# Optimization experiments

Measured on AMD Instinct MI355X. Metric: run time of the kernel, lower is better.

## Reference

```python
import jax, jax.numpy as jnp
import numpy as np
import math

NC = 80
STRIDES = [8.0, 16.0, 32.0]
BALANCE = [4.0, 1.0, 0.4]
BOX_W, OBJ_W, CLS_W = 7.5, 1.0, 0.5
B = 32
NT = 400


def build_targets(shapes, targets):
    """NumPy port of YOLOv11Loss.build_targets (na=1). Pure index/label
    construction -> depends only on shapes + ground-truth, no grads."""
    nt = targets.shape[0]
    ai = np.zeros((1, nt, 1), dtype=np.float32)  # na=1 anchor ids
    t_all = np.concatenate([targets[None].astype(np.float32), ai], axis=2)  # [1,nt,7]
    g = 0.5
    off = np.array([[0, 0], [1, 0], [0, 1], [-1, 0], [0, -1]], dtype=np.float32) * g
    out = []
    for i, shape in enumerate(shapes):
        anchor = float(STRIDES[i])
        H, W = shape[2], shape[3]
        gain = np.array([1, 1, W, H, W, H, 1], dtype=np.float32)
        t = t_all * gain  # [1,nt,7] in grid units
        r = t[..., 4:6] / anchor
        keep = np.maximum(r, 1.0 / r).max(axis=2) < 4.0  # [1,nt]
        t = t[keep]  # [n,7]
        gxy = t[:, 2:4]
        gxi = np.array([W, H], dtype=np.float32) - gxy
        jj, kk = ((gxy % 1 < g) & (gxy > 1)).T
        ll, mm = ((gxi % 1 < g) & (gxi > 1)).T
        J = np.stack([np.ones_like(jj), jj, kk, ll, mm])  # [5,n]
        t = np.tile(t[None], (5, 1, 1))[J]  # [m,7]
        offsets = (np.zeros_like(gxy)[None] + off[:, None])[J]  # [m,2]
        b = t[:, 0].astype(np.int64)
        c = t[:, 1].astype(np.int64)
        gxy = t[:, 2:4]
        gwh = t[:, 4:6]
        a = t[:, 6].astype(np.int64)
        gij = (gxy - offsets).astype(np.int64)  # trunc toward 0, matches .long()
        gi = np.clip(gij[:, 0], 0, W - 1)
        gj = np.clip(gij[:, 1], 0, H - 1)
        gij_c = np.stack([gi, gj], axis=1)  # torch clamps in-place before tbox
        tbox = np.concatenate([gxy - gij_c, gwh], axis=1).astype(np.float32)
        out.append((b, a, gj, gi, tbox, c))
    return out


def ciou(pbox, tbox, eps=1e-7):
    """Elementwise CIoU on [n,4] xywh boxes (matches bbox_iou(..., CIoU=True))."""
    px, py, pw, ph = pbox[:, 0], pbox[:, 1], pbox[:, 2], pbox[:, 3]
    tx, ty, tw, th = tbox[:, 0], tbox[:, 1], tbox[:, 2], tbox[:, 3]
    b1x1, b1x2 = px - pw / 2, px + pw / 2
    b1y1, b1y2 = py - ph / 2, py + ph / 2
    b2x1, b2x2 = tx - tw / 2, tx + tw / 2
    b2y1, b2y2 = ty - th / 2, ty + th / 2
    inter = jnp.clip(jnp.minimum(b1x2, b2x2) - jnp.maximum(b1x1, b2x1), 0) * \
            jnp.clip(jnp.minimum(b1y2, b2y2) - jnp.maximum(b1y1, b2y1), 0)
    union = pw * ph + tw * th - inter + eps
    iou = inter / union
    cw = jnp.maximum(b1x2, b2x2) - jnp.minimum(b1x1, b2x1)
    ch = jnp.maximum(b1y2, b2y2) - jnp.minimum(b1y1, b2y1)
    c2 = cw ** 2 + ch ** 2 + eps
    rho2 = ((b2x1 + b2x2 - b1x1 - b1x2) ** 2 + (b2y1 + b2y2 - b1y1 - b1y2) ** 2) / 4
    v = (4.0 / math.pi ** 2) * (jnp.arctan(tw / th) - jnp.arctan(pw / ph)) ** 2
    alpha = jax.lax.stop_gradient(v / (v - iou + (1 + eps)))
    return iou - (rho2 / c2 + v * alpha)


def bce_mean(logits, targets):
    # BCEWithLogitsLoss(pos_weight=1), mean reduction: softplus(x) - x*z
    return jnp.mean(jax.nn.softplus(logits) - logits * targets)


def setup_inputs() -> dict:
    key = jax.random.key(0)
    k0, k1, k2 = jax.random.split(key, 3)
    p0 = jax.random.normal(k0, (B, 1, 80, 80, NC + 5), dtype=jnp.float32)
    p1 = jax.random.normal(k1, (B, 1, 40, 40, NC + 5), dtype=jnp.float32)
    p2 = jax.random.normal(k2, (B, 1, 20, 20, NC + 5), dtype=jnp.float32)
    rng = np.random.default_rng(0)
    bidx = rng.integers(0, B, NT).astype(np.float32)
    cls = rng.integers(0, NC, NT).astype(np.float32)
    xy = rng.uniform(0.05, 0.95, (NT, 2)).astype(np.float32)
    wh = rng.uniform(0.05, 0.5, (NT, 2)).astype(np.float32)
    targets = jnp.asarray(np.concatenate([bidx[:, None], cls[:, None], xy, wh], axis=1))
    return {"p0": p0, "p1": p1, "p2": p2, "targets": targets}


def reference(p0, p1, p2, targets):
    preds = [p0, p1, p2]
    bt = build_targets([p.shape for p in preds], np.asarray(targets))
    lbox = jnp.zeros((), jnp.float32)
    lobj = jnp.zeros((), jnp.float32)
    lcls = jnp.zeros((), jnp.float32)
    for i, p in enumerate(preds):
        b, a, gj, gi, tb, tc = bt[i]
        tobj = jnp.zeros(p.shape[:4], p.dtype)
        n = b.shape[0]
        if n:
            pred = p[b, a, gj, gi]  # [n, nc+5] gather
            pxy = jax.nn.sigmoid(pred[:, :2]) * 2.0 - 0.5
            pwh = (jax.nn.sigmoid(pred[:, 2:4]) * 2.0) ** 2 * STRIDES[i]
            pbox = jnp.concatenate([pxy, pwh], axis=1)
            iou = ciou(pbox, jnp.asarray(tb))
            lbox = lbox + jnp.mean(1.0 - iou)
            iou_d = jax.lax.stop_gradient(jnp.clip(iou, 0.0)).astype(p.dtype)
            tobj = tobj.at[b, a, gj, gi].set(iou_d)  # scatter objectness targets
            pcls = pred[:, 5:]
            tmat = jnp.zeros((n, NC), p.dtype).at[np.arange(n), tc].set(1.0)
            lcls = lcls + bce_mean(pcls, tmat)
        lobj = lobj + bce_mean(p[..., 4], tobj) * BALANCE[i]
    lbox = lbox * BOX_W
    lobj = lobj * OBJ_W
    lcls = lcls * CLS_W
    bs = preds[0].shape[0]
    loss = (lbox + lobj + lcls) * bs
    comps = jax.lax.stop_gradient(jnp.stack([lbox, lobj, lcls]))
    return loss, comps
```

## Files before the change

### kernel.cpp

```cpp
#include <hip/hip_runtime.h>

#define NCLS 80
#define BATCH 32
#define N0 (BATCH * 80 * 80)
#define N1 (BATCH * 40 * 40)
#define N2 (BATCH * 20 * 20)
#define NCELL (N0 + N1 + N2)
#define NFLT (NCELL * (NCLS + 5))
#define NF4  (NFLT / 4)
#define L0F4 ((N0 * (NCLS + 5)) / 4)
#define L01F4 (((N0 + N1) * (NCLS + 5)) / 4)
#define TPB 256
#define WPB (TPB / 64)
#define STREAM_BLOCKS 2048
#define STRIDE4 (STREAM_BLOCKS * TPB)
#define NBMAX 2400

__device__ float g_part[NBMAX * 12];

__device__ __forceinline__ float sigmoid_f(float x) {
    return 1.0f / (1.0f + expf(-x));
}

__device__ __forceinline__ float softplus_f(float x) {
    return fmaxf(x, 0.0f) + log1pf(expf(-fabsf(x)));
}

__device__ __forceinline__ float ciou_f(float px, float py, float pw, float ph,
                                        float tx, float ty, float tw, float th) {
    const float eps = 1e-7f;
    float b1x1 = px - pw * 0.5f, b1x2 = px + pw * 0.5f;
    float b1y1 = py - ph * 0.5f, b1y2 = py + ph * 0.5f;
    float b2x1 = tx - tw * 0.5f, b2x2 = tx + tw * 0.5f;
    float b2y1 = ty - th * 0.5f, b2y2 = ty + th * 0.5f;
    float iw = fmaxf(fminf(b1x2, b2x2) - fmaxf(b1x1, b2x1), 0.0f);
    float ih = fmaxf(fminf(b1y2, b2y2) - fmaxf(b1y1, b2y1), 0.0f);
    float inter = iw * ih;
    float uni = pw * ph + tw * th - inter + eps;
    float iou = inter / uni;
    float cw = fmaxf(b1x2, b2x2) - fminf(b1x1, b2x1);
    float ch = fmaxf(b1y2, b2y2) - fminf(b1y1, b2y1);
    float c2 = cw * cw + ch * ch + eps;
    float dx = b2x1 + b2x2 - b1x1 - b1x2;
    float dy = b2y1 + b2y2 - b1y1 - b1y2;
    float rho2 = (dx * dx + dy * dy) * 0.25f;
    float dat = atanf(tw / th) - atanf(pw / ph);
    const float k = 0.40528473456935108577551785f;
    float v = k * dat * dat;
    float alpha = v / (v - iou + (1.0f + eps));
    return iou - (rho2 / c2 + v * alpha);
}

__device__ __forceinline__ void stream_body(
        const float4* __restrict__ f0, const float4* __restrict__ f1,
        const float4* __restrict__ f2, int i4, unsigned int r,
        float& acc0, float& acc1, float& acc2) {
    const float4* src;
    int off, lvl;
    if (i4 < L0F4)       { src = f0; off = i4;         lvl = 0; }
    else if (i4 < L01F4) { src = f1; off = i4 - L0F4;  lvl = 1; }
    else                 { src = f2; off = i4 - L01F4; lvl = 2; }
    float4 v = src[off];
    unsigned int j = 4u - r;
    float x = (j == 0u) ? v.x : (j == 1u) ? v.y : (j == 2u) ? v.z : v.w;
    float maskf = (r >= 1u && r <= 4u) ? 1.0f : 0.0f;
    float sp = maskf * softplus_f(x);
    acc0 += (lvl == 0) ? sp : 0.0f;
    acc1 += (lvl == 1) ? sp : 0.0f;
    acc2 += (lvl == 2) ? sp : 0.0f;
}

__global__ __launch_bounds__(TPB) void main_kernel(
        const float* __restrict__ p0,
        const float* __restrict__ p1,
        const float* __restrict__ p2,
        const float* __restrict__ tg, int nt, int tgtBlocks) {
    __shared__ float sh[12];
    int tid = threadIdx.x;
    if (tid < 12) sh[tid] = 0.0f;
    __syncthreads();

    if ((int)blockIdx.x >= tgtBlocks) {
        const float4* f0 = (const float4*)p0;
        const float4* f1 = (const float4*)p1;
        const float4* f2 = (const float4*)p2;
        int i4 = (blockIdx.x - tgtBlocks) * TPB + tid;
        unsigned int r = ((unsigned int)i4 * 4u) % 85u;
        float acc0 = 0.0f, acc1 = 0.0f, acc2 = 0.0f;
        while (i4 + 3 * STRIDE4 < NF4) {
            unsigned int r0 = r;
            unsigned int r1 = r0 + 32u; if (r1 >= 85u) r1 -= 85u;
            unsigned int r2 = r1 + 32u; if (r2 >= 85u) r2 -= 85u;
            unsigned int r3 = r2 + 32u; if (r3 >= 85u) r3 -= 85u;
            stream_body(f0, f1, f2, i4,               r0, acc0, acc1, acc2);
            stream_body(f0, f1, f2, i4 + STRIDE4,     r1, acc0, acc1, acc2);
            stream_body(f0, f1, f2, i4 + 2 * STRIDE4, r2, acc0, acc1, acc2);
            stream_body(f0, f1, f2, i4 + 3 * STRIDE4, r3, acc0, acc1, acc2);
            r = r3 + 32u; if (r >= 85u) r -= 85u;
            i4 += 4 * STRIDE4;
        }
        while (i4 < NF4) {
            stream_body(f0, f1, f2, i4, r, acc0, acc1, acc2);
            r += 32u; if (r >= 85u) r -= 85u;
            i4 += STRIDE4;
        }
        #pragma unroll
        for (int off = 32; off > 0; off >>= 1) {
            acc0 += __shfl_down(acc0, off, 64);
            acc1 += __shfl_down(acc1, off, 64);
            acc2 += __shfl_down(acc2, off, 64);
        }
        if ((tid & 63) == 0) {
            atomicAdd(&sh[9], acc0);
            atomicAdd(&sh[10], acc1);
            atomicAdd(&sh[11], acc2);
        }
    } else {
        int lane = tid & 63;
        int wtask = blockIdx.x * WPB + (tid >> 6);
        if (wtask < 3 * nt) {
            int lvl = wtask / nt;
            int t = wtask - lvl * nt;

            int W = (lvl == 0) ? 80 : ((lvl == 1) ? 40 : 20);
            float s = (lvl == 0) ? 8.0f : ((lvl == 1) ? 16.0f : 32.0f);
            const float* p = (lvl == 0) ? p0 : ((lvl == 1) ? p1 : p2);

            const float* row = tg + t * 6;
            float bf = row[0], cf = row[1];
            float x = row[2], y = row[3], w = row[4], h = row[5];

            float Wf = (float)W;
            float gw = w * Wf, gh = h * Wf;
            float rw = gw / s, rh = gh / s;
            float m = fmaxf(fmaxf(rw, 1.0f / rw), fmaxf(rh, 1.0f / rh));
            if (m < 4.0f) {
                float gx = x * Wf, gy = y * Wf;
                int b = (int)bf;
                int c = (int)cf;

                float ox[3], oy[3];
                int ne = 0;
                ox[ne] = 0.0f; oy[ne] = 0.0f; ne++;
                bool jj = (fmodf(gx, 1.0f) < 0.5f) && (gx > 1.0f);
                bool kk = (fmodf(gy, 1.0f) < 0.5f) && (gy > 1.0f);
                float gxi = Wf - gx, gyi = Wf - gy;
                bool ll = (fmodf(gxi, 1.0f) < 0.5f) && (gxi > 1.0f);
                bool mm = (fmodf(gyi, 1.0f) < 0.5f) && (gyi > 1.0f);
                if (jj) { ox[ne] = 0.5f;  oy[ne] = 0.0f;  ne++; }
                if (ll) { ox[ne] = -0.5f; oy[ne] = 0.0f;  ne++; }
                if (kk) { ox[ne] = 0.0f;  oy[ne] = 0.5f;  ne++; }
                if (mm) { ox[ne] = 0.0f;  oy[ne] = -0.5f; ne++; }

                float cls_lane = 0.0f;
                float lbox_u = 0.0f, lobj_u = 0.0f;
                int hot = 5 + c;
                for (int e = 0; e < ne; e++) {
                    int gi = (int)(gx - ox[e]);
                    int gj = (int)(gy - oy[e]);
                    gi = min(max(gi, 0), W - 1);
                    gj = min(max(gj, 0), W - 1);
                    int cell = (b * W + gj) * W + gi;
                    const float* pr = p + (size_t)cell * (NCLS + 5);

                    float v1 = pr[lane];
                    float v2 = (lane < 21) ? pr[64 + lane] : 0.0f;

                    float c0 = __shfl(v1, 0, 64);
                    float c1 = __shfl(v1, 1, 64);
                    float c2 = __shfl(v1, 2, 64);
                    float c3 = __shfl(v1, 3, 64);
                    float c4 = __shfl(v1, 4, 64);

                    float px = sigmoid_f(c0) * 2.0f - 0.5f;
                    float py = sigmoid_f(c1) * 2.0f - 0.5f;
                    float sw = sigmoid_f(c2) * 2.0f;
                    float shh = sigmoid_f(c3) * 2.0f;
                    float pw = sw * sw * s;
                    float ph = shh * shh * s;

                    float tbx = gx - (float)gi;
                    float tby = gy - (float)gj;

                    float iou = ciou_f(px, py, pw, ph, tbx, tby, gw, gh);
                    lbox_u += 1.0f - iou;
                    lobj_u += c4 * fmaxf(iou, 0.0f);

                    float s1 = (lane >= 5) ? softplus_f(v1) : 0.0f;
                    float s2 = (lane < 21) ? softplus_f(v2) : 0.0f;
                    cls_lane += s1 + s2;
                    if (hot < 64) { if (lane == hot)      cls_lane -= v1; }
                    else          { if (lane == hot - 64) cls_lane -= v2; }
                }
                #pragma unroll
                for (int off = 32; off > 0; off >>= 1)
                    cls_lane += __shfl_down(cls_lane, off, 64);
                if (lane == 0) {
                    atomicAdd(&sh[lvl], lbox_u);
                    atomicAdd(&sh[3 + lvl], cls_lane);
                    atomicAdd(&sh[6 + lvl], (float)ne);
                    atomicAdd(&sh[9 + lvl], -lobj_u);
                }
            }
        }
    }
    __syncthreads();
    if (tid < 12) g_part[blockIdx.x * 12 + tid] = sh[tid];
}

__global__ __launch_bounds__(TPB) void reduce_kernel(float* __restrict__ out,
                                                     int nblk) {
    __shared__ float red[12][TPB];
    int tid = threadIdx.x;
    float loc[12];
    #pragma unroll
    for (int c = 0; c < 12; c++) loc[c] = 0.0f;
    const float4* gp4 = (const float4*)g_part;
    for (int b = tid; b < nblk; b += TPB) {
        float4 a = gp4[b * 3];
        float4 bb = gp4[b * 3 + 1];
        float4 cc = gp4[b * 3 + 2];
        loc[0] += a.x;  loc[1] += a.y;  loc[2] += a.z;  loc[3] += a.w;
        loc[4] += bb.x; loc[5] += bb.y; loc[6] += bb.z; loc[7] += bb.w;
        loc[8] += cc.x; loc[9] += cc.y; loc[10] += cc.z; loc[11] += cc.w;
    }
    #pragma unroll
    for (int c = 0; c < 12; c++) red[c][tid] = loc[c];
    __syncthreads();
    for (int st = TPB / 2; st > 0; st >>= 1) {
        if (tid < st) {
            #pragma unroll
            for (int c = 0; c < 12; c++) red[c][tid] += red[c][tid + st];
        }
        __syncthreads();
    }
    if (tid == 0) {
        const float BAL[3] = {4.0f, 1.0f, 0.4f};
        const float NCF[3] = {(float)N0, (float)N1, (float)N2};
        float lbox = 0.0f, lcls = 0.0f, lobj = 0.0f;
        for (int l = 0; l < 3; l++) {
            float n = red[6 + l][0];
            if (n > 0.5f) {
                lbox += red[l][0] / n;
                lcls += red[3 + l][0] / (n * (float)NCLS);
            }
            lobj += red[9 + l][0] / NCF[l] * BAL[l];
        }
        lbox *= 7.5f;
        lcls *= 0.5f;
        float loss = (lbox + lobj + lcls) * (float)BATCH;
        out[0] = loss;
        out[1] = lbox;
        out[2] = lobj;
        out[3] = lcls;
    }
}

extern "C" void kernel_launch(void* const* d_in, const int* in_sizes, int n_in,
                              void* d_out, int out_size, void* d_ws, size_t ws_size,
                              hipStream_t stream) {
    const float* p0 = (const float*)d_in[0];
    const float* p1 = (const float*)d_in[1];
    const float* p2 = (const float*)d_in[2];
    const float* tg = (const float*)d_in[3];
    int nt = in_sizes[3] / 6;
    float* out = (float*)d_out;

    int nWaveTasks = 3 * nt;
    int tgtBlocks = (nWaveTasks + WPB - 1) / WPB;
    if (tgtBlocks > NBMAX - STREAM_BLOCKS) tgtBlocks = NBMAX - STREAM_BLOCKS;
    int nblk = tgtBlocks + STREAM_BLOCKS;

    main_kernel<<<nblk, TPB, 0, stream>>>(p0, p1, p2, tg, nt, tgtBlocks);
    reduce_kernel<<<1, TPB, 0, stream>>>(out, nblk);
}
```

Baseline: 128.2 us.

## Fuse final reduction into main kernel via last-block counter and deepen unroll

The separate single-block reduce kernel is removed. Each block now increments a global done counter after writing its partials, and the last block to finish performs the final 12-way reduction and resets the counter. This saves one kernel launch and its dependency gap. The streaming loop is also unrolled from 4 to 8 independent loads per iteration to keep more memory requests in flight. In exchange, every block pays for an extra atomic and fence, and the shared reduction array adds LDS use to every block, which may lower occupancy.

```diff
diff --git a/kernel.cpp b/kernel.cpp
--- a/kernel.cpp
+++ b/kernel.cpp
@@ -17,6 +17,7 @@
 #define NBMAX 2400
 
 __device__ float g_part[NBMAX * 12];
+__device__ int g_done;
 
 __device__ __forceinline__ float sigmoid_f(float x) {
     return 1.0f / (1.0f + expf(-x));
@@ -74,8 +75,10 @@
         const float* __restrict__ p0,
         const float* __restrict__ p1,
         const float* __restrict__ p2,
-        const float* __restrict__ tg, int nt, int tgtBlocks) {
+        const float* __restrict__ tg, int nt, int tgtBlocks, int nblk,
+        float* __restrict__ out) {
     __shared__ float sh[12];
+    __shared__ int lastFlag;
     int tid = threadIdx.x;
     if (tid < 12) sh[tid] = 0.0f;
     __syncthreads();
@@ -87,17 +90,20 @@
         int i4 = (blockIdx.x - tgtBlocks) * TPB + tid;
         unsigned int r = ((unsigned int)i4 * 4u) % 85u;
         float acc0 = 0.0f, acc1 = 0.0f, acc2 = 0.0f;
-        while (i4 + 3 * STRIDE4 < NF4) {
-            unsigned int r0 = r;
-            unsigned int r1 = r0 + 32u; if (r1 >= 85u) r1 -= 85u;
-            unsigned int r2 = r1 + 32u; if (r2 >= 85u) r2 -= 85u;
-            unsigned int r3 = r2 + 32u; if (r3 >= 85u) r3 -= 85u;
-            stream_body(f0, f1, f2, i4,               r0, acc0, acc1, acc2);
-            stream_body(f0, f1, f2, i4 + STRIDE4,     r1, acc0, acc1, acc2);
-            stream_body(f0, f1, f2, i4 + 2 * STRIDE4, r2, acc0, acc1, acc2);
-            stream_body(f0, f1, f2, i4 + 3 * STRIDE4, r3, acc0, acc1, acc2);
-            r = r3 + 32u; if (r >= 85u) r -= 85u;
-            i4 += 4 * STRIDE4;
+        while (i4 + 7 * STRIDE4 < NF4) {
+            unsigned int rr[8];
+            rr[0] = r;
+            #pragma unroll
+            for (int u = 1; u < 8; u++) {
+                rr[u] = rr[u - 1] + 32u;
+                if (rr[u] >= 85u) rr[u] -= 85u;
+            }
+            #pragma unroll
+            for (int u = 0; u < 8; u++)
+                stream_body(f0, f1, f2, i4 + u * STRIDE4, rr[u],
+                            acc0, acc1, acc2);
+            r = rr[7] + 32u; if (r >= 85u) r -= 85u;
+            i4 += 8 * STRIDE4;
         }
         while (i4 < NF4) {
             stream_body(f0, f1, f2, i4, r, acc0, acc1, acc2);
@@ -206,12 +212,17 @@
     }
     __syncthreads();
     if (tid < 12) g_part[blockIdx.x * 12 + tid] = sh[tid];
-}
-
-__global__ __launch_bounds__(TPB) void reduce_kernel(float* __restrict__ out,
-                                                     int nblk) {
+
+    if (tid == 0) {
+        __threadfence();
+        int old = atomicAdd(&g_done, 1);
+        lastFlag = (old == nblk - 1);
+    }
+    __syncthreads();
+    if (!lastFlag) return;
+    __threadfence();
+
     __shared__ float red[12][TPB];
-    int tid = threadIdx.x;
     float loc[12];
     #pragma unroll
     for (int c = 0; c < 12; c++) loc[c] = 0.0f;
@@ -253,6 +264,7 @@
         out[1] = lbox;
         out[2] = lobj;
         out[3] = lcls;
+        g_done = 0;
     }
 }
 
@@ -271,6 +283,6 @@
     if (tgtBlocks > NBMAX - STREAM_BLOCKS) tgtBlocks = NBMAX - STREAM_BLOCKS;
     int nblk = tgtBlocks + STREAM_BLOCKS;
 
-    main_kernel<<<nblk, TPB, 0, stream>>>(p0, p1, p2, tg, nt, tgtBlocks);
-    reduce_kernel<<<1, TPB, 0, stream>>>(out, nblk);
-}
+    main_kernel<<<nblk, TPB, 0, stream>>>(p0, p1, p2, tg, nt, tgtBlocks, nblk,
+                                          out);
+}
```

Result: slower. 205.0 us (+59.9%).

## Gather only objectness logits instead of streaming the whole prediction tensor

Applied to the files above, without the earlier changes.

Replaces the grid-stride float4 stream over every prediction value, where only channel 4 was used, with one thread per grid cell that loads just the objectness logit at stride 85. It then applies softplus, does a wave reduction and adds the result to that level's shared accumulator. This is meant to cut DRAM traffic, since only the cache lines holding objectness values are fetched. In exchange the loads are strided and uncoalesced, and the grid size is now fixed by the cell count. NBMAX is lowered to fit the new block count.

```diff
diff --git a/kernel.cpp b/kernel.cpp
--- a/kernel.cpp
+++ b/kernel.cpp
@@ -5,16 +5,12 @@
 #define N0 (BATCH * 80 * 80)
 #define N1 (BATCH * 40 * 40)
 #define N2 (BATCH * 20 * 20)
-#define NCELL (N0 + N1 + N2)
-#define NFLT (NCELL * (NCLS + 5))
-#define NF4  (NFLT / 4)
-#define L0F4 ((N0 * (NCLS + 5)) / 4)
-#define L01F4 (((N0 + N1) * (NCLS + 5)) / 4)
 #define TPB 256
 #define WPB (TPB / 64)
-#define STREAM_BLOCKS 2048
-#define STRIDE4 (STREAM_BLOCKS * TPB)
-#define NBMAX 2400
+#define OBJ_BLOCKS ((N0 + N1 + N2) / TPB)
+#define OBJ_B0 (N0 / TPB)
+#define OBJ_B01 ((N0 + N1) / TPB)
+#define NBMAX 1500
 
 __device__ float g_part[NBMAX * 12];
 
@@ -51,25 +47,6 @@
     return iou - (rho2 / c2 + v * alpha);
 }
 
-__device__ __forceinline__ void stream_body(
-        const float4* __restrict__ f0, const float4* __restrict__ f1,
-        const float4* __restrict__ f2, int i4, unsigned int r,
-        float& acc0, float& acc1, float& acc2) {
-    const float4* src;
-    int off, lvl;
-    if (i4 < L0F4)       { src = f0; off = i4;         lvl = 0; }
-    else if (i4 < L01F4) { src = f1; off = i4 - L0F4;  lvl = 1; }
-    else                 { src = f2; off = i4 - L01F4; lvl = 2; }
-    float4 v = src[off];
-    unsigned int j = 4u - r;
-    float x = (j == 0u) ? v.x : (j == 1u) ? v.y : (j == 2u) ? v.z : v.w;
-    float maskf = (r >= 1u && r <= 4u) ? 1.0f : 0.0f;
-    float sp = maskf * softplus_f(x);
-    acc0 += (lvl == 0) ? sp : 0.0f;
-    acc1 += (lvl == 1) ? sp : 0.0f;
-    acc2 += (lvl == 2) ? sp : 0.0f;
-}
-
 __global__ __launch_bounds__(TPB) void main_kernel(
         const float* __restrict__ p0,
         const float* __restrict__ p1,
@@ -81,40 +58,19 @@
     __syncthreads();
 
     if ((int)blockIdx.x >= tgtBlocks) {
-        const float4* f0 = (const float4*)p0;
-        const float4* f1 = (const float4*)p1;
-        const float4* f2 = (const float4*)p2;
-        int i4 = (blockIdx.x - tgtBlocks) * TPB + tid;
-        unsigned int r = ((unsigned int)i4 * 4u) % 85u;
-        float acc0 = 0.0f, acc1 = 0.0f, acc2 = 0.0f;
-        while (i4 + 3 * STRIDE4 < NF4) {
-            unsigned int r0 = r;
-            unsigned int r1 = r0 + 32u; if (r1 >= 85u) r1 -= 85u;
-            unsigned int r2 = r1 + 32u; if (r2 >= 85u) r2 -= 85u;
-            unsigned int r3 = r2 + 32u; if (r3 >= 85u) r3 -= 85u;
-            stream_body(f0, f1, f2, i4,               r0, acc0, acc1, acc2);
-            stream_body(f0, f1, f2, i4 + STRIDE4,     r1, acc0, acc1, acc2);
-            stream_body(f0, f1, f2, i4 + 2 * STRIDE4, r2, acc0, acc1, acc2);
-            stream_body(f0, f1, f2, i4 + 3 * STRIDE4, r3, acc0, acc1, acc2);
-            r = r3 + 32u; if (r >= 85u) r -= 85u;
-            i4 += 4 * STRIDE4;
-        }
-        while (i4 < NF4) {
-            stream_body(f0, f1, f2, i4, r, acc0, acc1, acc2);
-            r += 32u; if (r >= 85u) r -= 85u;
-            i4 += STRIDE4;
-        }
+        int ob = blockIdx.x - tgtBlocks;
+        int lvl, cb;
+        const float* p;
+        if (ob < OBJ_B0)       { lvl = 0; cb = ob;            p = p0; }
+        else if (ob < OBJ_B01) { lvl = 1; cb = ob - OBJ_B0;   p = p1; }
+        else                   { lvl = 2; cb = ob - OBJ_B01;  p = p2; }
+        int cell = cb * TPB + tid;
+        float xo = p[(size_t)cell * (NCLS + 5) + 4];
+        float v = softplus_f(xo);
         #pragma unroll
-        for (int off = 32; off > 0; off >>= 1) {
-            acc0 += __shfl_down(acc0, off, 64);
-            acc1 += __shfl_down(acc1, off, 64);
-            acc2 += __shfl_down(acc2, off, 64);
-        }
-        if ((tid & 63) == 0) {
-            atomicAdd(&sh[9], acc0);
-            atomicAdd(&sh[10], acc1);
-            atomicAdd(&sh[11], acc2);
-        }
+        for (int off = 32; off > 0; off >>= 1)
+            v += __shfl_down(v, off, 64);
+        if ((tid & 63) == 0) atomicAdd(&sh[9 + lvl], v);
     } else {
         int lane = tid & 63;
         int wtask = blockIdx.x * WPB + (tid >> 6);
@@ -268,8 +224,8 @@
 
     int nWaveTasks = 3 * nt;
     int tgtBlocks = (nWaveTasks + WPB - 1) / WPB;
-    if (tgtBlocks > NBMAX - STREAM_BLOCKS) tgtBlocks = NBMAX - STREAM_BLOCKS;
-    int nblk = tgtBlocks + STREAM_BLOCKS;
+    if (tgtBlocks > NBMAX - OBJ_BLOCKS) tgtBlocks = NBMAX - OBJ_BLOCKS;
+    int nblk = tgtBlocks + OBJ_BLOCKS;
 
     main_kernel<<<nblk, TPB, 0, stream>>>(p0, p1, p2, tg, nt, tgtBlocks);
     reduce_kernel<<<1, TPB, 0, stream>>>(out, nblk);
```

Result: faster. 117.2 us (-8.6%).
